# Kernel tuning notes

Measured on AMD Instinct MI355X. Metric: run time of the kernel, lower is better.

## Reference

```python
import jax, jax.numpy as jnp
import numpy as np

TAU = 32.0
ALPHA = 0.9
B, C, F = 4096, 512, 128  # batch, n_classes, n_bits


def setup_inputs() -> dict:
    key = jax.random.key(0)
    k1, k2, k3, k4 = jax.random.split(key, 4)
    X = jax.random.normal(k1, (B, F), dtype=jnp.float32)
    T = jax.random.randint(k2, (B, C), 0, 2).astype(jnp.int32)  # 0/1 multi-label
    # kaiming_normal_(mode='fan_out') on a [C, F] tensor -> std = sqrt(2 / C)
    std = np.sqrt(2.0 / C).astype(np.float32)
    means = jax.random.normal(k3, (C, F), dtype=jnp.float32) * std
    log_vars = jax.random.normal(k4, (C, F), dtype=jnp.float32) * std
    return {"X": X, "T": T, "means": means, "log_vars": log_vars}


def _l2_normalize(x, eps=1e-12):
    # matches torch F.normalize(p=2): x / max(||x||, eps)
    n = jnp.sqrt(jnp.sum(x * x, axis=-1, keepdims=True))
    return x / jnp.maximum(n, eps)


def _mahalanobis(Xn, mu, log_vars):
    # M[i,j] = sum_f (x_if - mu_jf)^2 / exp(lv_jf)
    # expanded into three GEMM-like terms -> never materializes [N,C,F]
    inv = jnp.exp(-log_vars)                         # [C, F]
    t1 = (Xn * Xn) @ inv.T                           # [N, C]
    t2 = Xn @ (mu * inv).T                           # [N, C]
    t3 = jnp.sum(mu * mu * inv, axis=-1)             # [C]
    return t1 - 2.0 * t2 + t3[None, :]


def reference(X, T, means, log_vars):
    lv = jnp.clip(log_vars, 0.0, 6.0)                # relu6
    Xn = _l2_normalize(X)
    mu = _l2_normalize(means)
    D = _mahalanobis(Xn, mu, lv)                     # [N, C]

    P_all = jax.nn.softmax(-TAU * D, axis=1)         # [N, C]
    Tf = T.astype(X.dtype)
    P_sum = jnp.sum(P_all * Tf, axis=1)              # [N]
    nz = P_sum != 0
    safe = jnp.where(nz, P_sum, 1.0)
    loss = -jnp.sum(jnp.where(nz, jnp.log(safe), 0.0)) / jnp.maximum(
        jnp.sum(nz).astype(X.dtype), 1.0)

    # classes present in the batch (concrete mask -> static column selection)
    cw = np.asarray(jnp.sum(T, axis=0) != 0)
    Dc = D[:, cw]                                    # [N, Ccw]
    Tc = Tf[:, cw]
    S = Tc + jnp.exp(-ALPHA * Dc) * (1.0 - Tc)
    return (loss, S)
```

## Files before the change

kernel.cpp:

```cpp
#include <hip/hip_runtime.h>
#include <hip/hip_bf16.h>
#include <math.h>

#define NB 4096
#define NC 512
#define NF 128
#define NK 256
#define TAUc 32.0f
#define ALPHAc 0.9f

typedef __attribute__((ext_vector_type(8))) short bf16x8;
typedef __attribute__((ext_vector_type(4))) float f32x4;
typedef __attribute__((address_space(1))) const unsigned int gu32;
typedef __attribute__((address_space(3))) unsigned int lu32;

__device__ inline void splitbf(float x, short& hi, short& lo) {
  unsigned u = __float_as_uint(x);
  hi = (short)(u >> 16);
  float l = x - __uint_as_float(u & 0xFFFF0000u);
  lo = (short)(__float_as_uint(l) >> 16);
}

__global__ __launch_bounds__(128) void k_prepB(const float* __restrict__ means,
                                               const float* __restrict__ logv,
                                               ushort* __restrict__ Bh,
                                               ushort* __restrict__ Bl,
                                               float* __restrict__ t3) {
  __shared__ float p2[2];
  __shared__ float q2[2];
  int c = blockIdx.x, f = threadIdx.x;
  float mu = means[(size_t)c * NF + f];
  float lv = fminf(fmaxf(logv[(size_t)c * NF + f], 0.f), 6.f);
  float iv = __expf(-lv);
  float s = mu * mu;
  #pragma unroll
  for (int o = 1; o < 64; o <<= 1) s += __shfl_xor(s, o, 64);
  if ((f & 63) == 0) p2[f >> 6] = s;
  __syncthreads();
  float mun = mu / fmaxf(sqrtf(p2[0] + p2[1]), 1e-12f);

  int ct = c >> 4, lr = c & 15;
  auto swadr = [&](int k) {
    return (size_t)(ct * 8 + (k >> 5)) * 512 + ((k >> 3) & 3) * 128 + lr * 8 + (k & 7);
  };
  short h, l;
  splitbf(iv, h, l);
  size_t a1 = swadr(f);
  Bh[a1] = (ushort)h; Bl[a1] = (ushort)l;
  splitbf(-2.f * mun * iv, h, l);
  size_t a2 = swadr(f + NF);
  Bh[a2] = (ushort)h; Bl[a2] = (ushort)l;

  float t = mun * mun * iv;
  #pragma unroll
  for (int o = 1; o < 64; o <<= 1) t += __shfl_xor(t, o, 64);
  if ((f & 63) == 0) q2[f >> 6] = t;
  __syncthreads();
  if (f == 0) t3[c] = q2[0] + q2[1];
}

__global__ __launch_bounds__(512) void k_zero(int* __restrict__ colnz) {
  colnz[threadIdx.x] = 0;
}

__global__ __launch_bounds__(256) void k_mask(const int* __restrict__ T,
                                              int* __restrict__ colnz) {
  int r0 = blockIdx.x * 16;
  int a0 = 0, a1 = 0;
  for (int r = 0; r < 16; ++r) {
    const int* row = T + (size_t)(r0 + r) * NC;
    a0 |= row[threadIdx.x];
    a1 |= row[threadIdx.x + 256];
  }
  if (a0) atomicOr(colnz + threadIdx.x, 1);
  if (a1) atomicOr(colnz + threadIdx.x + 256, 1);
}

__global__ __launch_bounds__(512) void k_scan(const int* __restrict__ colnz,
                                              int* __restrict__ pos) {
  __shared__ int s[NC];
  int t = threadIdx.x;
  int f = colnz[t] ? 1 : 0;
  s[t] = f;
  __syncthreads();
  for (int o = 1; o < NC; o <<= 1) {
    int add = (t >= o) ? s[t - o] : 0;
    __syncthreads();
    s[t] += add;
    __syncthreads();
  }
  pos[t] = s[t] - f;
}

__global__ __launch_bounds__(512) void k_fused(const float* __restrict__ X,
                                               const int* __restrict__ T,
                                               const ushort* __restrict__ Bh,
                                               const ushort* __restrict__ Bl,
                                               const float* __restrict__ t3,
                                               const int* __restrict__ colnz,
                                               const int* __restrict__ pos,
                                               float* __restrict__ Sout,
                                               float* __restrict__ rowm,
                                               float* __restrict__ rowz,
                                               float* __restrict__ rowp,
                                               int Csel, int ident) {
  __shared__ __align__(16) unsigned char smB[131072];
  __shared__ float partm[2][64], partz[2][64], partp[2][64];
  int tid = threadIdx.x;
  int lane = tid & 63, w = tid >> 6;
  int wm = w & 3, wn = w >> 2;
  int lr = lane & 15, kq = lane >> 4;
  int bx = blockIdx.x;
  int gc = bx & 3, gr = bx >> 2;
  int r0 = gr * 64, c0 = gc * 128;

  {
    const ushort* gh = Bh + (size_t)gc * 32768;
    const ushort* gl = Bl + (size_t)gc * 32768;
    #pragma unroll
    for (int s = 0; s < 8; ++s) {
      unsigned lo = (unsigned)(s * 8192 + w * 1024);
      size_t ge = (size_t)(s * 512 + w * 64 + lane) * 8;
      __builtin_amdgcn_global_load_lds((gu32*)(gh + ge), (lu32*)(smB + lo), 16, 0, 0);
      __builtin_amdgcn_global_load_lds((gu32*)(gl + ge), (lu32*)(smB + 65536 + lo), 16, 0, 0);
    }
  }

  bf16x8 Afh[8], Afl[8];
  {
    float xv[4][8];
    float rsum = 0.f;
    const float* xrow = X + (size_t)(r0 + wm * 16 + lr) * NF + 8 * kq;
    #pragma unroll
    for (int c = 0; c < 4; ++c) {
      float4 u0 = *(const float4*)(xrow + 32 * c);
      float4 u1 = *(const float4*)(xrow + 32 * c + 4);
      xv[c][0] = u0.x; xv[c][1] = u0.y; xv[c][2] = u0.z; xv[c][3] = u0.w;
      xv[c][4] = u1.x; xv[c][5] = u1.y; xv[c][6] = u1.z; xv[c][7] = u1.w;
      #pragma unroll
      for (int j = 0; j < 8; ++j) rsum = fmaf(xv[c][j], xv[c][j], rsum);
    }
    rsum += __shfl_xor(rsum, 16, 64);
    rsum += __shfl_xor(rsum, 32, 64);
    float rn = 1.0f / fmaxf(sqrtf(rsum), 1e-12f);
    #pragma unroll
    for (int c = 0; c < 4; ++c) {
      #pragma unroll
      for (int j = 0; j < 8; ++j) {
        float xn = xv[c][j] * rn;
        short h, l;
        splitbf(xn * xn, h, l);
        Afh[c][j] = h; Afl[c][j] = l;
        splitbf(xn, h, l);
        Afh[c + 4][j] = h; Afl[c + 4][j] = l;
      }
    }
  }

  int tfv[4][4];
  #pragma unroll
  for (int i = 0; i < 4; ++i) {
    const int* tr = T + (size_t)(r0 + wm * 16 + 4 * kq + i) * NC + c0 + wn * 64 + lr;
    #pragma unroll
    for (int t = 0; t < 4; ++t) tfv[t][i] = tr[16 * t];
  }

  __syncthreads();

  f32x4 acc[4] = {};
  #pragma unroll
  for (int k8 = 0; k8 < 8; ++k8) {
    #pragma unroll
    for (int t = 0; t < 4; ++t) {
      unsigned off = (unsigned)((((wn * 4 + t) * 8 + k8) * 64 + lane) * 16);
      bf16x8 bh = *(const bf16x8*)(smB + off);
      bf16x8 bl = *(const bf16x8*)(smB + 65536 + off);
      acc[t] = __builtin_amdgcn_mfma_f32_16x16x32_bf16(Afh[k8], bh, acc[t], 0, 0, 0);
      acc[t] = __builtin_amdgcn_mfma_f32_16x16x32_bf16(Afl[k8], bh, acc[t], 0, 0, 0);
      acc[t] = __builtin_amdgcn_mfma_f32_16x16x32_bf16(Afh[k8], bl, acc[t], 0, 0, 0);
    }
  }

  float d[4][4];
  #pragma unroll
  for (int t = 0; t < 4; ++t) {
    float tt = t3[c0 + wn * 64 + 16 * t + lr];
    #pragma unroll
    for (int i = 0; i < 4; ++i) d[t][i] = acc[t][i] + tt;
  }

  float m4[4], Zi[4], Pi[4];
  #pragma unroll
  for (int i = 0; i < 4; ++i) {
    float mm = fminf(fminf(d[0][i], d[1][i]), fminf(d[2][i], d[3][i]));
    #pragma unroll
    for (int o = 1; o < 16; o <<= 1) mm = fminf(mm, __shfl_xor(mm, o, 64));
    float Z = 0.f, P = 0.f;
    #pragma unroll
    for (int t = 0; t < 4; ++t) {
      float p = __expf(TAUc * (mm - d[t][i]));
      Z += p;
      if (tfv[t][i]) P += p;
    }
    #pragma unroll
    for (int o = 1; o < 16; o <<= 1) { Z += __shfl_xor(Z, o, 64); P += __shfl_xor(P, o, 64); }
    m4[i] = mm; Zi[i] = Z; Pi[i] = P;
  }

  if (ident) {
    #pragma unroll
    for (int i = 0; i < 4; ++i) {
      float* srow = Sout + (size_t)(r0 + wm * 16 + 4 * kq + i) * NC + c0 + wn * 64 + lr;
      #pragma unroll
      for (int t = 0; t < 4; ++t)
        srow[16 * t] = tfv[t][i] ? 1.0f : __expf(-ALPHAc * d[t][i]);
    }
  } else {
    #pragma unroll
    for (int i = 0; i < 4; ++i) {
      float* srow = Sout + (size_t)(r0 + wm * 16 + 4 * kq + i) * Csel;
      #pragma unroll
      for (int t = 0; t < 4; ++t) {
        int c = c0 + wn * 64 + 16 * t + lr;
        if (colnz[c]) srow[pos[c]] = tfv[t][i] ? 1.0f : __expf(-ALPHAc * d[t][i]);
      }
    }
  }

  if (lr == 0) {
    #pragma unroll
    for (int i = 0; i < 4; ++i) {
      int row = wm * 16 + 4 * kq + i;
      partm[wn][row] = m4[i];
      partz[wn][row] = Zi[i];
      partp[wn][row] = Pi[i];
    }
  }
  __syncthreads();
  if (tid < 64) {
    float m0 = partm[0][tid], m1 = partm[1][tid];
    float m = fminf(m0, m1);
    float e0 = __expf(TAUc * (m - m0)), e1 = __expf(TAUc * (m - m1));
    int g = (r0 + tid) * 4 + gc;
    rowm[g] = m;
    rowz[g] = partz[0][tid] * e0 + partz[1][tid] * e1;
    rowp[g] = partp[0][tid] * e0 + partp[1][tid] * e1;
  }
}

__global__ __launch_bounds__(1024) void k_fin(const float* __restrict__ rowm,
                                              const float* __restrict__ rowz,
                                              const float* __restrict__ rowp,
                                              float* __restrict__ out) {
  __shared__ float sl[16];
  __shared__ int sc[16];
  int tid = threadIdx.x;
  int lane = tid & 63, w = tid >> 6;
  float ls = 0.f; int lc = 0;
  for (int r = tid; r < NB; r += 1024) {
    float4 mv = ((const float4*)rowm)[r];
    float4 zv = ((const float4*)rowz)[r];
    float4 pv = ((const float4*)rowp)[r];
    float m = fminf(fminf(mv.x, mv.y), fminf(mv.z, mv.w));
    float e0 = __expf(TAUc * (m - mv.x));
    float e1 = __expf(TAUc * (m - mv.y));
    float e2 = __expf(TAUc * (m - mv.z));
    float e3 = __expf(TAUc * (m - mv.w));
    float Z = zv.x * e0 + zv.y * e1 + zv.z * e2 + zv.w * e3;
    float P = pv.x * e0 + pv.y * e1 + pv.z * e2 + pv.w * e3;
    float Ps = P / Z;
    if (Ps > 0.f) { ls += logf(Ps); ++lc; }
  }
  #pragma unroll
  for (int o = 1; o < 64; o <<= 1) { ls += __shfl_xor(ls, o, 64); lc += __shfl_xor(lc, o, 64); }
  if (lane == 0) { sl[w] = ls; sc[w] = lc; }
  __syncthreads();
  if (tid == 0) {
    float s = 0.f; int c = 0;
    #pragma unroll
    for (int i = 0; i < 16; ++i) { s += sl[i]; c += sc[i]; }
    out[0] = -s / fmaxf((float)c, 1.0f);
  }
}

extern "C" void kernel_launch(void* const* d_in, const int* in_sizes, int n_in,
                              void* d_out, int out_size, void* d_ws, size_t ws_size,
                              hipStream_t stream) {
  const float* X     = (const float*)d_in[0];
  const int*   T     = (const int*)d_in[1];
  const float* means = (const float*)d_in[2];
  const float* logv  = (const float*)d_in[3];
  float* out = (float*)d_out;
  char* ws = (char*)d_ws;

  ushort* Bh   = (ushort*)(ws);
  ushort* Bl   = (ushort*)(ws + 262144);
  float*  t3   = (float*) (ws + 524288);
  float*  rowm = (float*) (ws + 526336);
  float*  rowz = (float*) (ws + 591872);
  float*  rowp = (float*) (ws + 657408);
  int*    colnz= (int*)   (ws + 722944);
  int*    pos  = (int*)   (ws + 724992);

  int Csel = (out_size - 1) / NB;
  int ident = (Csel == NC);

  k_prepB<<<NC, NF, 0, stream>>>(means, logv, Bh, Bl, t3);
  if (!ident) {
    k_zero<<<1, NC, 0, stream>>>(colnz);
    k_mask<<<NB / 16, 256, 0, stream>>>(T, colnz);
    k_scan<<<1, NC, 0, stream>>>(colnz, pos);
  }
  k_fused<<<256, 512, 0, stream>>>(X, T, Bh, Bl, t3, colnz, pos,
                                   out + 1, rowm, rowz, rowp, Csel, ident);
  k_fin<<<1, 1024, 0, stream>>>(rowm, rowz, rowp, out);
}
```

Measured before the change: 23.87 us.

## Fuse class-parameter preprocessing into main kernel, dropping the prepB launch

```diff
diff --git a/kernel.cpp b/kernel.cpp
--- a/kernel.cpp
+++ b/kernel.cpp
@@ -11,52 +11,12 @@
 
 typedef __attribute__((ext_vector_type(8))) short bf16x8;
 typedef __attribute__((ext_vector_type(4))) float f32x4;
-typedef __attribute__((address_space(1))) const unsigned int gu32;
-typedef __attribute__((address_space(3))) unsigned int lu32;
 
 __device__ inline void splitbf(float x, short& hi, short& lo) {
   unsigned u = __float_as_uint(x);
   hi = (short)(u >> 16);
   float l = x - __uint_as_float(u & 0xFFFF0000u);
   lo = (short)(__float_as_uint(l) >> 16);
-}
-
-__global__ __launch_bounds__(128) void k_prepB(const float* __restrict__ means,
-                                               const float* __restrict__ logv,
-                                               ushort* __restrict__ Bh,
-                                               ushort* __restrict__ Bl,
-                                               float* __restrict__ t3) {
-  __shared__ float p2[2];
-  __shared__ float q2[2];
-  int c = blockIdx.x, f = threadIdx.x;
-  float mu = means[(size_t)c * NF + f];
-  float lv = fminf(fmaxf(logv[(size_t)c * NF + f], 0.f), 6.f);
-  float iv = __expf(-lv);
-  float s = mu * mu;
-  #pragma unroll
-  for (int o = 1; o < 64; o <<= 1) s += __shfl_xor(s, o, 64);
-  if ((f & 63) == 0) p2[f >> 6] = s;
-  __syncthreads();
-  float mun = mu / fmaxf(sqrtf(p2[0] + p2[1]), 1e-12f);
-
-  int ct = c >> 4, lr = c & 15;
-  auto swadr = [&](int k) {
-    return (size_t)(ct * 8 + (k >> 5)) * 512 + ((k >> 3) & 3) * 128 + lr * 8 + (k & 7);
-  };
-  short h, l;
-  splitbf(iv, h, l);
-  size_t a1 = swadr(f);
-  Bh[a1] = (ushort)h; Bl[a1] = (ushort)l;
-  splitbf(-2.f * mun * iv, h, l);
-  size_t a2 = swadr(f + NF);
-  Bh[a2] = (ushort)h; Bl[a2] = (ushort)l;
-
-  float t = mun * mun * iv;
-  #pragma unroll
-  for (int o = 1; o < 64; o <<= 1) t += __shfl_xor(t, o, 64);
-  if ((f & 63) == 0) q2[f >> 6] = t;
-  __syncthreads();
-  if (f == 0) t3[c] = q2[0] + q2[1];
 }
 
 __global__ __launch_bounds__(512) void k_zero(int* __restrict__ colnz) {
@@ -94,9 +54,8 @@
 
 __global__ __launch_bounds__(512) void k_fused(const float* __restrict__ X,
                                                const int* __restrict__ T,
-                                               const ushort* __restrict__ Bh,
-                                               const ushort* __restrict__ Bl,
-                                               const float* __restrict__ t3,
+                                               const float* __restrict__ means,
+                                               const float* __restrict__ logv,
                                                const int* __restrict__ colnz,
                                                const int* __restrict__ pos,
                                                float* __restrict__ Sout,
@@ -105,6 +64,7 @@
                                                float* __restrict__ rowp,
                                                int Csel, int ident) {
   __shared__ __align__(16) unsigned char smB[131072];
+  __shared__ float t3s[128];
   __shared__ float partm[2][64], partz[2][64], partp[2][64];
   int tid = threadIdx.x;
   int lane = tid & 63, w = tid >> 6;
@@ -114,22 +74,22 @@
   int gc = bx & 3, gr = bx >> 2;
   int r0 = gr * 64, c0 = gc * 128;
 
+  int cls = w * 16 + (lane >> 2);
+  int q = lane & 3;
+  int c15 = (lane >> 2) & 15;
+  float mua[32], lva[32];
   {
-    const ushort* gh = Bh + (size_t)gc * 32768;
-    const ushort* gl = Bl + (size_t)gc * 32768;
-    #pragma unroll
-    for (int s = 0; s < 8; ++s) {
-      unsigned lo = (unsigned)(s * 8192 + w * 1024);
-      size_t ge = (size_t)(s * 512 + w * 64 + lane) * 8;
-      __builtin_amdgcn_global_load_lds((gu32*)(gh + ge), (lu32*)(smB + lo), 16, 0, 0);
-      __builtin_amdgcn_global_load_lds((gu32*)(gl + ge), (lu32*)(smB + 65536 + lo), 16, 0, 0);
-    }
-  }
-
-  bf16x8 Afh[8], Afl[8];
+    const float4* mp = (const float4*)(means + (size_t)(c0 + cls) * NF + 32 * q);
+    const float4* lp = (const float4*)(logv + (size_t)(c0 + cls) * NF + 32 * q);
+    #pragma unroll
+    for (int i = 0; i < 8; ++i) {
+      *(float4*)(mua + 4 * i) = mp[i];
+      *(float4*)(lva + 4 * i) = lp[i];
+    }
+  }
+
+  float xv[4][8];
   {
-    float xv[4][8];
-    float rsum = 0.f;
     const float* xrow = X + (size_t)(r0 + wm * 16 + lr) * NF + 8 * kq;
     #pragma unroll
     for (int c = 0; c < 4; ++c) {
@@ -137,9 +97,58 @@
       float4 u1 = *(const float4*)(xrow + 32 * c + 4);
       xv[c][0] = u0.x; xv[c][1] = u0.y; xv[c][2] = u0.z; xv[c][3] = u0.w;
       xv[c][4] = u1.x; xv[c][5] = u1.y; xv[c][6] = u1.z; xv[c][7] = u1.w;
+    }
+  }
+  int tfv[4][4];
+  #pragma unroll
+  for (int i = 0; i < 4; ++i) {
+    const int* tr = T + (size_t)(r0 + wm * 16 + 4 * kq + i) * NC + c0 + wn * 64 + lr;
+    #pragma unroll
+    for (int t = 0; t < 4; ++t) tfv[t][i] = tr[16 * t];
+  }
+
+  {
+    float s = 0.f;
+    #pragma unroll
+    for (int k = 0; k < 32; ++k) s = fmaf(mua[k], mua[k], s);
+    s += __shfl_xor(s, 1, 64);
+    s += __shfl_xor(s, 2, 64);
+    float rn_c = 1.0f / fmaxf(sqrtf(s), 1e-12f);
+    float t3a = 0.f;
+    #pragma unroll
+    for (int i8 = 0; i8 < 4; ++i8) {
+      bf16x8 h1, l1, h2, l2;
+      #pragma unroll
+      for (int j = 0; j < 8; ++j) {
+        int jj = i8 * 8 + j;
+        float ivv = __expf(-fminf(fmaxf(lva[jj], 0.f), 6.f));
+        float m = mua[jj] * rn_c;
+        short h, l;
+        splitbf(ivv, h, l);
+        h1[j] = h; l1[j] = l;
+        splitbf(-2.f * m * ivv, h, l);
+        h2[j] = h; l2[j] = l;
+        t3a = fmaf(m * m, ivv, t3a);
+      }
+      unsigned e1 = (unsigned)((w * 8 + q) * 512 + i8 * 128 + c15 * 8) * 2u;
+      unsigned e2 = (unsigned)((w * 8 + 4 + q) * 512 + i8 * 128 + c15 * 8) * 2u;
+      *(bf16x8*)(smB + e1) = h1;
+      *(bf16x8*)(smB + 65536 + e1) = l1;
+      *(bf16x8*)(smB + e2) = h2;
+      *(bf16x8*)(smB + 65536 + e2) = l2;
+    }
+    t3a += __shfl_xor(t3a, 1, 64);
+    t3a += __shfl_xor(t3a, 2, 64);
+    if (q == 0) t3s[cls] = t3a;
+  }
+
+  bf16x8 Afh[8], Afl[8];
+  {
+    float rsum = 0.f;
+    #pragma unroll
+    for (int c = 0; c < 4; ++c)
       #pragma unroll
       for (int j = 0; j < 8; ++j) rsum = fmaf(xv[c][j], xv[c][j], rsum);
-    }
     rsum += __shfl_xor(rsum, 16, 64);
     rsum += __shfl_xor(rsum, 32, 64);
     float rn = 1.0f / fmaxf(sqrtf(rsum), 1e-12f);
@@ -157,14 +166,6 @@
     }
   }
 
-  int tfv[4][4];
-  #pragma unroll
-  for (int i = 0; i < 4; ++i) {
-    const int* tr = T + (size_t)(r0 + wm * 16 + 4 * kq + i) * NC + c0 + wn * 64 + lr;
-    #pragma unroll
-    for (int t = 0; t < 4; ++t) tfv[t][i] = tr[16 * t];
-  }
-
   __syncthreads();
 
   f32x4 acc[4] = {};
@@ -184,7 +185,7 @@
   float d[4][4];
   #pragma unroll
   for (int t = 0; t < 4; ++t) {
-    float tt = t3[c0 + wn * 64 + 16 * t + lr];
+    float tt = t3s[wn * 64 + 16 * t + lr];
     #pragma unroll
     for (int i = 0; i < 4; ++i) d[t][i] = acc[t][i] + tt;
   }
@@ -293,25 +294,21 @@
   float* out = (float*)d_out;
   char* ws = (char*)d_ws;
 
-  ushort* Bh   = (ushort*)(ws);
-  ushort* Bl   = (ushort*)(ws + 262144);
-  float*  t3   = (float*) (ws + 524288);
-  float*  rowm = (float*) (ws + 526336);
-  float*  rowz = (float*) (ws + 591872);
-  float*  rowp = (float*) (ws + 657408);
-  int*    colnz= (int*)   (ws + 722944);
-  int*    pos  = (int*)   (ws + 724992);
+  float*  rowm = (float*) (ws);
+  float*  rowz = (float*) (ws + 65536);
+  float*  rowp = (float*) (ws + 131072);
+  int*    colnz= (int*)   (ws + 196608);
+  int*    pos  = (int*)   (ws + 198656);
 
   int Csel = (out_size - 1) / NB;
   int ident = (Csel == NC);
 
-  k_prepB<<<NC, NF, 0, stream>>>(means, logv, Bh, Bl, t3);
   if (!ident) {
     k_zero<<<1, NC, 0, stream>>>(colnz);
     k_mask<<<NB / 16, 256, 0, stream>>>(T, colnz);
     k_scan<<<1, NC, 0, stream>>>(colnz, pos);
   }
-  k_fused<<<256, 512, 0, stream>>>(X, T, Bh, Bl, t3, colnz, pos,
+  k_fused<<<256, 512, 0, stream>>>(X, T, means, logv, colnz, pos,
                                    out + 1, rowm, rowz, rowp, Csel, ident);
   k_fin<<<1, 1024, 0, stream>>>(rowm, rowz, rowp, out);
 }
```

Result: faster. 22.12 us, median of 2 (-7.3%).
